# Performance work log

Hardware: AMD Instinct MI355X
Metric: run time of the kernel (lower is better)

Reference implementation:

```python
import jax, jax.numpy as jnp
import numpy as np

B, P = 16, 20480          # scenes, points per scene
N = B * P
FEAT, HID = 128, 128      # FP output channels, head hidden width
CIN = FEAT + 3            # 131 = xyz + features (hard-coded in source: view(..., 131))
GRIPPER_DEPTH = 0.1034
HEADS = (("s", 1), ("z1", 3), ("z2", 3), ("w", 1))


def setup_inputs() -> dict:
    key = jax.random.key(0)
    ks = jax.random.split(key, 2 + 2 * len(HEADS))
    inp = {
        "point_feat": jax.random.normal(ks[0], (N, FEAT), jnp.float32),
        "points": jax.random.normal(ks[1], (N, 3), jnp.float32) * 0.3,
        "batch": jnp.repeat(jnp.arange(B, dtype=jnp.int32), P),
    }
    i = 2
    for name, od in HEADS:
        inp[f"W1_{name}"] = jax.random.normal(ks[i], (HID, CIN), jnp.float32) / np.sqrt(CIN).astype(np.float32)
        inp[f"b1_{name}"] = jnp.zeros((HID,), jnp.float32)
        inp[f"W2_{name}"] = jax.random.normal(ks[i + 1], (od, HID), jnp.float32) / np.sqrt(HID).astype(np.float32)
        inp[f"b2_{name}"] = jnp.zeros((od,), jnp.float32)
        i += 2
    return inp


def _head(x, W1, b1, W2, b2):
    # 1x1 Conv1d stack == per-point MLP: [N,CIN] -> [N,out]
    h = jax.nn.relu(x @ W1.T + b1)
    return h @ W2.T + b2


def _norm(v):
    return v / jnp.linalg.norm(v, axis=1, keepdims=True)


def _forward(point_feat, points,
             W1_s, b1_s, W2_s, b2_s,
             W1_z1, b1_z1, W2_z1, b2_z1,
             W1_z2, b1_z2, W2_z2, b2_z2,
             W1_w, b1_w, W2_w, b2_w):
    pf = jnp.concatenate([points, point_feat], axis=1)          # [N,131]
    s = _head(pf, W1_s, b1_s, W2_s, b2_s)                        # [N,1] (logits)
    z1 = _head(pf, W1_z1, b1_z1, W2_z1, b2_z1)                   # [N,3]
    z2 = _head(pf, W1_z2, b1_z2, W2_z2, b2_z2)                   # [N,3]
    w = _head(pf, W1_w, b1_w, W2_w, b2_w)                        # [N,1]

    # forward() post-processing
    z1 = _norm(z1)
    z2 = z2 - jnp.sum(z1 * z2, axis=-1, keepdims=True) * z1
    z2 = _norm(z2)
    w = jnp.clip(w, -0.08, 0.08)

    # build_6d_grasps, vectorized over all N points
    base = _norm(z1)
    inner = jnp.sum(base * z2, axis=1, keepdims=True)
    approach = (z2 - inner * base) / jnp.linalg.norm(z2, axis=1, keepdims=True)
    base_n = _norm(base)                                          # column 0
    app_n = _norm(approach)                                       # column 2
    grasp_y = _norm(jnp.cross(app_n, base_n))                     # column 1
    trans = points - GRIPPER_DEPTH * app_n + (w / 2.0) * base_n   # column 3
    top = jnp.stack([base_n, grasp_y, app_n, trans], axis=2)      # [N,3,4]
    bottom = jnp.broadcast_to(jnp.array([0.0, 0.0, 0.0, 1.0], jnp.float32), (top.shape[0], 1, 4))
    grasps = jnp.concatenate([top, bottom], axis=1)               # [N,4,4]

    pts_out = points.reshape(B, P, 3)
    grasps_out = grasps.reshape(B, P, 4, 4)
    s_out = s.reshape(B, P)
    w_out = jax.nn.relu(w).reshape(B, P)
    feats_out = pf.reshape(B, P, CIN)
    return pts_out, grasps_out, s_out, w_out, feats_out


def reference(point_feat, points, batch,
              W1_s, b1_s, W2_s, b2_s,
              W1_z1, b1_z1, W2_z1, b2_z1,
              W1_z2, b1_z2, W2_z2, b2_z2,
              W1_w, b1_w, W2_w, b2_w):
    # batch ids only determine num_batches = max(batch)+1 = B (static here)
    return _forward(point_feat, points,
                    W1_s, b1_s, W2_s, b2_s,
                    W1_z1, b1_z1, W2_z1, b2_z1,
                    W1_z2, b1_z2, W2_z2, b2_z2,
                    W1_w, b1_w, W2_w, b2_w)
```

## Files before the change

### kernel.cpp

```cpp
#include <hip/hip_runtime.h>

#define NPTS (16*20480)
#define BM 32
#define NTILES (NPTS/BM)

typedef _Float16 f16;
typedef _Float16 f16x8 __attribute__((ext_vector_type(8)));
typedef float    f32x4 __attribute__((ext_vector_type(4)));

#define O_PTS   ((size_t)0)
#define O_GRASP ((size_t)NPTS*3)
#define O_S     (O_GRASP + (size_t)NPTS*16)
#define O_W     (O_S + (size_t)NPTS)
#define O_FEAT  (O_W + (size_t)NPTS)

struct Params {
  const float* point_feat;
  const float* points;
  const float* W1[4];
  const float* b1[4];
  const float* W2[4];
  const float* b2[4];
  float* out;
};

__launch_bounds__(512, 2)
__global__ void contactnet_fused(Params P)
{
  __shared__ float pf32[BM][132];
  __shared__ float h32[BM][548];
  __shared__ float W2s[8][132];
  __shared__ float b2s[8];
  __shared__ float out2[BM][8][2];
  __shared__ float gr[BM][16];

  const int t    = threadIdx.x;
  const int lane = t & 63;
  const int wv   = t >> 6;
  const int head = wv >> 1;
  const int half = wv & 1;
  const int l15  = lane & 15;
  const int lg   = lane >> 4;

  for (int i = t; i < 8*128; i += 512) {
    int o = i >> 7, k = i & 127;
    int hd = (o + 2) / 3;
    int r  = o - (hd ? 3*hd - 2 : 0);
    W2s[o][k] = P.W2[hd][r*128 + k];
  }
  if (t < 8) {
    int o = t, hd = (o + 2) / 3, r = o - (hd ? 3*hd - 2 : 0);
    b2s[o] = P.b2[hd][r];
  }

  float bias1[4];
  float w1x[4], w1y[4], w1z[4];
  f16x8 Wf_hi[4][4];
  f16x8 Wf_lo[4][4];
  {
    const float* W1h = P.W1[head];
    const float* b1h = P.b1[head];
    #pragma unroll
    for (int nt = 0; nt < 4; ++nt) {
      int row = half*64 + nt*16 + l15;
      const float* wr = W1h + row*131;
      bias1[nt] = b1h[row];
      w1x[nt] = wr[0]; w1y[nt] = wr[1]; w1z[nt] = wr[2];
      #pragma unroll
      for (int kk = 0; kk < 4; ++kk) {
        f16x8 fh, fl;
        int k0 = 3 + kk*32 + lg*8;
        #pragma unroll
        for (int j = 0; j < 8; ++j) {
          float w = wr[k0 + j];
          f16 hi = (f16)w;
          fh[j] = hi;
          fl[j] = (f16)(w - (float)hi);
        }
        Wf_hi[nt][kk] = fh;
        Wf_lo[nt][kk] = fl;
      }
    }
  }

  for (int tile = blockIdx.x; tile < NTILES; tile += gridDim.x) {
    const int base = tile * BM;

    #pragma unroll
    for (int r = 0; r < 2; ++r) {
      int f = t + r*512;
      int p = f >> 5, c4 = f & 31;
      const f32x4 v = *(const f32x4*)(P.point_feat + ((size_t)(base+p)*128 + c4*4));
      *(f32x4*)&pf32[p][c4*4] = v;
      float* dst = P.out + O_FEAT + (size_t)(base+p)*131 + 3 + c4*4;
      dst[0] = v[0]; dst[1] = v[1]; dst[2] = v[2]; dst[3] = v[3];
    }
    if (t < 96) {
      int p = t / 3, c = t - p*3;
      float v = P.points[(size_t)base*3 + t];
      pf32[p][128 + c] = v;
      P.out[O_PTS + (size_t)base*3 + t] = v;
      P.out[O_FEAT + (size_t)(base+p)*131 + c] = v;
    }
    __syncthreads();

    f32x4 acc[2][4];
    #pragma unroll
    for (int mt = 0; mt < 2; ++mt)
      #pragma unroll
      for (int nt = 0; nt < 4; ++nt) {
        acc[mt][nt][0] = bias1[nt]; acc[mt][nt][1] = bias1[nt];
        acc[mt][nt][2] = bias1[nt]; acc[mt][nt][3] = bias1[nt];
      }

    #pragma unroll
    for (int mt = 0; mt < 2; ++mt)
      #pragma unroll
      for (int r = 0; r < 4; ++r) {
        int m = mt*16 + lg*4 + r;
        float x = pf32[m][128], y = pf32[m][129], z = pf32[m][130];
        #pragma unroll
        for (int nt = 0; nt < 4; ++nt)
          acc[mt][nt][r] += x*w1x[nt] + y*w1y[nt] + z*w1z[nt];
      }

    #pragma unroll
    for (int kk = 0; kk < 4; ++kk) {
      f16x8 ah[2], al[2];
      #pragma unroll
      for (int mt = 0; mt < 2; ++mt) {
        int m  = mt*16 + l15;
        int k0 = kk*32 + lg*8;
        f32x4 v0 = *(const f32x4*)&pf32[m][k0];
        f32x4 v1 = *(const f32x4*)&pf32[m][k0+4];
        f16x8 h_, l_;
        #pragma unroll
        for (int j = 0; j < 4; ++j) {
          f16 hi = (f16)v0[j];
          h_[j] = hi; l_[j] = (f16)(v0[j] - (float)hi);
        }
        #pragma unroll
        for (int j = 0; j < 4; ++j) {
          f16 hi = (f16)v1[j];
          h_[4+j] = hi; l_[4+j] = (f16)(v1[j] - (float)hi);
        }
        ah[mt] = h_; al[mt] = l_;
      }
      #pragma unroll
      for (int mt = 0; mt < 2; ++mt)
        #pragma unroll
        for (int nt = 0; nt < 4; ++nt) {
          acc[mt][nt] = __builtin_amdgcn_mfma_f32_16x16x32_f16(ah[mt], Wf_hi[nt][kk], acc[mt][nt], 0, 0, 0);
          acc[mt][nt] = __builtin_amdgcn_mfma_f32_16x16x32_f16(al[mt], Wf_hi[nt][kk], acc[mt][nt], 0, 0, 0);
          acc[mt][nt] = __builtin_amdgcn_mfma_f32_16x16x32_f16(ah[mt], Wf_lo[nt][kk], acc[mt][nt], 0, 0, 0);
        }
    }

    #pragma unroll
    for (int mt = 0; mt < 2; ++mt)
      #pragma unroll
      for (int nt = 0; nt < 4; ++nt)
        #pragma unroll
        for (int r = 0; r < 4; ++r) {
          int prow = mt*16 + lg*4 + r;
          h32[prow][head*136 + half*64 + nt*16 + l15] = fmaxf(acc[mt][nt][r], 0.f);
        }
    __syncthreads();

    {
      int kh = t >> 8;
      int p  = (t >> 3) & 31;
      int o  = t & 7;
      int hd = (o + 2) / 3;
      float a2 = kh ? 0.f : b2s[o];
      const float* hp = &h32[p][hd*136 + kh*64];
      const float* wp = &W2s[o][kh*64];
      #pragma unroll
      for (int i = 0; i < 16; ++i) {
        f32x4 hv = *(const f32x4*)(hp + i*4);
        f32x4 wv = *(const f32x4*)(wp + i*4);
        a2 = fmaf(hv[0], wv[0], a2);
        a2 = fmaf(hv[1], wv[1], a2);
        a2 = fmaf(hv[2], wv[2], a2);
        a2 = fmaf(hv[3], wv[3], a2);
      }
      out2[p][o][kh] = a2;
    }
    __syncthreads();

    if (t < BM) {
      const int p = t;
      float s   = out2[p][0][0] + out2[p][0][1];
      float z1x = out2[p][1][0] + out2[p][1][1];
      float z1y = out2[p][2][0] + out2[p][2][1];
      float z1z = out2[p][3][0] + out2[p][3][1];
      float z2x = out2[p][4][0] + out2[p][4][1];
      float z2y = out2[p][5][0] + out2[p][5][1];
      float z2z = out2[p][6][0] + out2[p][6][1];
      float w   = out2[p][7][0] + out2[p][7][1];
      float px = pf32[p][128], py = pf32[p][129], pz = pf32[p][130];

      float n1 = sqrtf(z1x*z1x + z1y*z1y + z1z*z1z);
      z1x /= n1; z1y /= n1; z1z /= n1;
      float d12 = z1x*z2x + z1y*z2y + z1z*z2z;
      z2x -= d12*z1x; z2y -= d12*z1y; z2z -= d12*z1z;
      float n2 = sqrtf(z2x*z2x + z2y*z2y + z2z*z2z);
      z2x /= n2; z2y /= n2; z2z /= n2;
      w = fminf(fmaxf(w, -0.08f), 0.08f);

      float nb = sqrtf(z1x*z1x + z1y*z1y + z1z*z1z);
      float bx = z1x/nb, by = z1y/nb, bz = z1z/nb;
      float inner = bx*z2x + by*z2y + bz*z2z;
      float na2 = sqrtf(z2x*z2x + z2y*z2y + z2z*z2z);
      float ax = (z2x - inner*bx)/na2, ay = (z2y - inner*by)/na2, az = (z2z - inner*bz)/na2;
      float nbn = sqrtf(bx*bx + by*by + bz*bz);
      float bnx = bx/nbn, bny = by/nbn, bnz = bz/nbn;
      float nan2 = sqrtf(ax*ax + ay*ay + az*az);
      float anx = ax/nan2, any_ = ay/nan2, anz = az/nan2;
      float cx = any_*bnz - anz*bny;
      float cy = anz*bnx - anx*bnz;
      float cz = anx*bny - any_*bnx;
      float nc = sqrtf(cx*cx + cy*cy + cz*cz);
      float gx = cx/nc, gyv = cy/nc, gzv = cz/nc;
      float tx = px - 0.1034f*anx + 0.5f*w*bnx;
      float ty = py - 0.1034f*any_ + 0.5f*w*bny;
      float tz = pz - 0.1034f*anz + 0.5f*w*bnz;

      gr[p][0]=bnx; gr[p][1]=gx;  gr[p][2]=anx;  gr[p][3]=tx;
      gr[p][4]=bny; gr[p][5]=gyv; gr[p][6]=any_; gr[p][7]=ty;
      gr[p][8]=bnz; gr[p][9]=gzv; gr[p][10]=anz; gr[p][11]=tz;
      gr[p][12]=0.f; gr[p][13]=0.f; gr[p][14]=0.f; gr[p][15]=1.f;

      P.out[O_S + base + p] = s;
      P.out[O_W + base + p] = fmaxf(w, 0.f);
    }
    __syncthreads();

    P.out[O_GRASP + (size_t)base*16 + t] = gr[t >> 4][t & 15];
    __syncthreads();
  }
}

extern "C" void kernel_launch(void* const* d_in, const int* in_sizes, int n_in,
                              void* d_out, int out_size, void* d_ws, size_t ws_size,
                              hipStream_t stream) {
  Params P;
  P.point_feat = (const float*)d_in[0];
  P.points     = (const float*)d_in[1];
  int idx = 3;
  for (int h = 0; h < 4; ++h) {
    P.W1[h] = (const float*)d_in[idx + 0];
    P.b1[h] = (const float*)d_in[idx + 1];
    P.W2[h] = (const float*)d_in[idx + 2];
    P.b2[h] = (const float*)d_in[idx + 3];
    idx += 4;
  }
  P.out = (float*)d_out;
  contactnet_fused<<<dim3(512), dim3(512), 0, stream>>>(P);
}
```

Measured before the change: 537.6 us.

## Double-buffer tiles, prefetch next tile, fuse second layer via shuffle reductions

Restructures the fused MLP kernel to 1024-thread blocks on a 256-block grid, with each wave owning 32 hidden units of one head. The next tile's features and points are prefetched from global memory into registers while the current tile is computed, then written into a double-buffered shared f16 hi/lo split. The second layer is computed in registers from the MFMA accumulators with cross-lane shuffle reductions, which removes the shared hidden-activation buffer and one barrier per tile. The costs are higher register pressure under the 1024-thread launch bound, fewer resident blocks, and added shuffle traffic.

```diff
diff --git a/kernel.cpp b/kernel.cpp
--- a/kernel.cpp
+++ b/kernel.cpp
@@ -3,8 +3,10 @@
 #define NPTS (16*20480)
 #define BM 32
 #define NTILES (NPTS/BM)
+#define GRID 256
 
 typedef _Float16 f16;
+typedef _Float16 f16x4 __attribute__((ext_vector_type(4)));
 typedef _Float16 f16x8 __attribute__((ext_vector_type(8)));
 typedef float    f32x4 __attribute__((ext_vector_type(4)));
 
@@ -24,106 +26,113 @@
   float* out;
 };
 
-__launch_bounds__(512, 2)
+__launch_bounds__(1024, 4)
 __global__ void contactnet_fused(Params P)
 {
-  __shared__ float pf32[BM][132];
-  __shared__ float h32[BM][548];
-  __shared__ float W2s[8][132];
+  __shared__ f16   afh[2][BM][136];
+  __shared__ f16   afl[2][BM][136];
+  __shared__ float xyzs[2][BM][3];
+  __shared__ float out2[BM][33];
+  __shared__ float gr[BM][16];
   __shared__ float b2s[8];
-  __shared__ float out2[BM][8][2];
-  __shared__ float gr[BM][16];
 
   const int t    = threadIdx.x;
   const int lane = t & 63;
   const int wv   = t >> 6;
-  const int head = wv >> 1;
-  const int half = wv & 1;
+  const int head = wv >> 2;
+  const int q    = wv & 3;
   const int l15  = lane & 15;
   const int lg   = lane >> 4;
 
-  for (int i = t; i < 8*128; i += 512) {
-    int o = i >> 7, k = i & 127;
-    int hd = (o + 2) / 3;
-    int r  = o - (hd ? 3*hd - 2 : 0);
-    W2s[o][k] = P.W2[hd][r*128 + k];
-  }
-  if (t < 8) {
-    int o = t, hd = (o + 2) / 3, r = o - (hd ? 3*hd - 2 : 0);
-    b2s[o] = P.b2[hd][r];
-  }
-
-  float bias1[4];
-  float w1x[4], w1y[4], w1z[4];
-  f16x8 Wf_hi[4][4];
-  f16x8 Wf_lo[4][4];
+  if (t < 8) { int o = t, hd = (o + 2) / 3, r = o - (hd ? 3*hd - 2 : 0); b2s[o] = P.b2[hd][r]; }
+
+  float bias1[2], w1x[2], w1y[2], w1z[2];
+  f16x8 Whi[2][4], Wlo[2][4];
   {
     const float* W1h = P.W1[head];
     const float* b1h = P.b1[head];
     #pragma unroll
-    for (int nt = 0; nt < 4; ++nt) {
-      int row = half*64 + nt*16 + l15;
+    for (int nt = 0; nt < 2; ++nt) {
+      int row = q*32 + nt*16 + l15;
       const float* wr = W1h + row*131;
       bias1[nt] = b1h[row];
       w1x[nt] = wr[0]; w1y[nt] = wr[1]; w1z[nt] = wr[2];
       #pragma unroll
       for (int kk = 0; kk < 4; ++kk) {
         f16x8 fh, fl;
-        int k0 = 3 + kk*32 + lg*8;
         #pragma unroll
         for (int j = 0; j < 8; ++j) {
-          float w = wr[k0 + j];
+          float w = wr[3 + kk*32 + lg*8 + j];
           f16 hi = (f16)w;
-          fh[j] = hi;
-          fl[j] = (f16)(w - (float)hi);
+          fh[j] = hi; fl[j] = (f16)(w - (float)hi);
         }
-        Wf_hi[nt][kk] = fh;
-        Wf_lo[nt][kk] = fl;
-      }
-    }
-  }
-
-  for (int tile = blockIdx.x; tile < NTILES; tile += gridDim.x) {
+        Whi[nt][kk] = fh; Wlo[nt][kk] = fl;
+      }
+    }
+  }
+  const int goff = (head==0) ? 0 : (head==1) ? 1 : (head==2) ? 4 : 7;
+  const int od   = (head==1 || head==2) ? 3 : 1;
+  float W2r[3][2];
+  #pragma unroll
+  for (int ol = 0; ol < 3; ++ol)
+    #pragma unroll
+    for (int nt = 0; nt < 2; ++nt)
+      W2r[ol][nt] = (ol < od) ? P.W2[head][ol*128 + q*32 + nt*16 + l15] : 0.f;
+
+  const int p_  = t >> 5;
+  const int c4_ = t & 31;
+
+  int tile = blockIdx.x;
+  {
+    f32x4 v = *(const f32x4*)(P.point_feat + ((size_t)(tile*BM + p_)*128 + c4_*4));
+    float xv = (t < 96) ? P.points[(size_t)tile*BM*3 + t] : 0.f;
+    f16x4 hs, ls;
+    #pragma unroll
+    for (int j = 0; j < 4; ++j) { f16 hi = (f16)v[j]; hs[j] = hi; ls[j] = (f16)(v[j] - (float)hi); }
+    *(f16x4*)&afh[0][p_][c4_*4] = hs;
+    *(f16x4*)&afl[0][p_][c4_*4] = ls;
+    float* dst = P.out + O_FEAT + (size_t)(tile*BM + p_)*131 + 3 + c4_*4;
+    dst[0] = v[0]; dst[1] = v[1]; dst[2] = v[2]; dst[3] = v[3];
+    if (t < 96) {
+      int pp = t / 3, c = t - pp*3;
+      xyzs[0][pp][c] = xv;
+      P.out[O_PTS + (size_t)tile*BM*3 + t] = xv;
+      P.out[O_FEAT + (size_t)(tile*BM + pp)*131 + c] = xv;
+    }
+  }
+  __syncthreads();
+
+  int cur = 0;
+  for (;;) {
     const int base = tile * BM;
-
-    #pragma unroll
-    for (int r = 0; r < 2; ++r) {
-      int f = t + r*512;
-      int p = f >> 5, c4 = f & 31;
-      const f32x4 v = *(const f32x4*)(P.point_feat + ((size_t)(base+p)*128 + c4*4));
-      *(f32x4*)&pf32[p][c4*4] = v;
-      float* dst = P.out + O_FEAT + (size_t)(base+p)*131 + 3 + c4*4;
-      dst[0] = v[0]; dst[1] = v[1]; dst[2] = v[2]; dst[3] = v[3];
-    }
-    if (t < 96) {
-      int p = t / 3, c = t - p*3;
-      float v = P.points[(size_t)base*3 + t];
-      pf32[p][128 + c] = v;
-      P.out[O_PTS + (size_t)base*3 + t] = v;
-      P.out[O_FEAT + (size_t)(base+p)*131 + c] = v;
-    }
-    __syncthreads();
-
-    f32x4 acc[2][4];
+    const int nxt  = tile + GRID;
+    const bool has = (nxt < NTILES);
+
+    f32x4 pv = {0,0,0,0};
+    float pxyz = 0.f;
+    if (has) {
+      pv = *(const f32x4*)(P.point_feat + ((size_t)(nxt*BM + p_)*128 + c4_*4));
+      if (t < 96) pxyz = P.points[(size_t)nxt*BM*3 + t];
+    }
+
+    f32x4 acc[2][2];
     #pragma unroll
     for (int mt = 0; mt < 2; ++mt)
       #pragma unroll
-      for (int nt = 0; nt < 4; ++nt) {
+      for (int nt = 0; nt < 2; ++nt) {
         acc[mt][nt][0] = bias1[nt]; acc[mt][nt][1] = bias1[nt];
         acc[mt][nt][2] = bias1[nt]; acc[mt][nt][3] = bias1[nt];
       }
-
     #pragma unroll
     for (int mt = 0; mt < 2; ++mt)
       #pragma unroll
       for (int r = 0; r < 4; ++r) {
         int m = mt*16 + lg*4 + r;
-        float x = pf32[m][128], y = pf32[m][129], z = pf32[m][130];
-        #pragma unroll
-        for (int nt = 0; nt < 4; ++nt)
+        float x = xyzs[cur][m][0], y = xyzs[cur][m][1], z = xyzs[cur][m][2];
+        #pragma unroll
+        for (int nt = 0; nt < 2; ++nt)
           acc[mt][nt][r] += x*w1x[nt] + y*w1y[nt] + z*w1z[nt];
       }
-
     #pragma unroll
     for (int kk = 0; kk < 4; ++kk) {
       f16x8 ah[2], al[2];
@@ -131,74 +140,68 @@
       for (int mt = 0; mt < 2; ++mt) {
         int m  = mt*16 + l15;
         int k0 = kk*32 + lg*8;
-        f32x4 v0 = *(const f32x4*)&pf32[m][k0];
-        f32x4 v1 = *(const f32x4*)&pf32[m][k0+4];
-        f16x8 h_, l_;
-        #pragma unroll
-        for (int j = 0; j < 4; ++j) {
-          f16 hi = (f16)v0[j];
-          h_[j] = hi; l_[j] = (f16)(v0[j] - (float)hi);
+        ah[mt] = *(const f16x8*)&afh[cur][m][k0];
+        al[mt] = *(const f16x8*)&afl[cur][m][k0];
+      }
+      #pragma unroll
+      for (int mt = 0; mt < 2; ++mt)
+        #pragma unroll
+        for (int nt = 0; nt < 2; ++nt) {
+          acc[mt][nt] = __builtin_amdgcn_mfma_f32_16x16x32_f16(ah[mt], Whi[nt][kk], acc[mt][nt], 0, 0, 0);
+          acc[mt][nt] = __builtin_amdgcn_mfma_f32_16x16x32_f16(al[mt], Whi[nt][kk], acc[mt][nt], 0, 0, 0);
+          acc[mt][nt] = __builtin_amdgcn_mfma_f32_16x16x32_f16(ah[mt], Wlo[nt][kk], acc[mt][nt], 0, 0, 0);
         }
-        #pragma unroll
-        for (int j = 0; j < 4; ++j) {
-          f16 hi = (f16)v1[j];
-          h_[4+j] = hi; l_[4+j] = (f16)(v1[j] - (float)hi);
-        }
-        ah[mt] = h_; al[mt] = l_;
-      }
-      #pragma unroll
-      for (int mt = 0; mt < 2; ++mt)
-        #pragma unroll
-        for (int nt = 0; nt < 4; ++nt) {
-          acc[mt][nt] = __builtin_amdgcn_mfma_f32_16x16x32_f16(ah[mt], Wf_hi[nt][kk], acc[mt][nt], 0, 0, 0);
-          acc[mt][nt] = __builtin_amdgcn_mfma_f32_16x16x32_f16(al[mt], Wf_hi[nt][kk], acc[mt][nt], 0, 0, 0);
-          acc[mt][nt] = __builtin_amdgcn_mfma_f32_16x16x32_f16(ah[mt], Wf_lo[nt][kk], acc[mt][nt], 0, 0, 0);
-        }
-    }
-
-    #pragma unroll
-    for (int mt = 0; mt < 2; ++mt)
-      #pragma unroll
-      for (int nt = 0; nt < 4; ++nt)
-        #pragma unroll
-        for (int r = 0; r < 4; ++r) {
-          int prow = mt*16 + lg*4 + r;
-          h32[prow][head*136 + half*64 + nt*16 + l15] = fmaxf(acc[mt][nt][r], 0.f);
-        }
-    __syncthreads();
-
-    {
-      int kh = t >> 8;
-      int p  = (t >> 3) & 31;
-      int o  = t & 7;
-      int hd = (o + 2) / 3;
-      float a2 = kh ? 0.f : b2s[o];
-      const float* hp = &h32[p][hd*136 + kh*64];
-      const float* wp = &W2s[o][kh*64];
-      #pragma unroll
-      for (int i = 0; i < 16; ++i) {
-        f32x4 hv = *(const f32x4*)(hp + i*4);
-        f32x4 wv = *(const f32x4*)(wp + i*4);
-        a2 = fmaf(hv[0], wv[0], a2);
-        a2 = fmaf(hv[1], wv[1], a2);
-        a2 = fmaf(hv[2], wv[2], a2);
-        a2 = fmaf(hv[3], wv[3], a2);
-      }
-      out2[p][o][kh] = a2;
+    }
+
+    #pragma unroll
+    for (int ol = 0; ol < 3; ++ol) {
+      if (ol < od) {
+        #pragma unroll
+        for (int mt = 0; mt < 2; ++mt)
+          #pragma unroll
+          for (int r = 0; r < 4; ++r) {
+            float v = 0.f;
+            #pragma unroll
+            for (int nt = 0; nt < 2; ++nt)
+              v = fmaf(W2r[ol][nt], fmaxf(acc[mt][nt][r], 0.f), v);
+            v += __shfl_xor(v, 1);
+            v += __shfl_xor(v, 2);
+            v += __shfl_xor(v, 4);
+            v += __shfl_xor(v, 8);
+            if (l15 == 0)
+              out2[mt*16 + lg*4 + r][(goff + ol)*4 + q] = v;
+          }
+      }
+    }
+
+    if (has) {
+      f16x4 hs, ls;
+      #pragma unroll
+      for (int j = 0; j < 4; ++j) { f16 hi = (f16)pv[j]; hs[j] = hi; ls[j] = (f16)(pv[j] - (float)hi); }
+      *(f16x4*)&afh[cur^1][p_][c4_*4] = hs;
+      *(f16x4*)&afl[cur^1][p_][c4_*4] = ls;
+      float* dst = P.out + O_FEAT + (size_t)(nxt*BM + p_)*131 + 3 + c4_*4;
+      dst[0] = pv[0]; dst[1] = pv[1]; dst[2] = pv[2]; dst[3] = pv[3];
+      if (t < 96) {
+        int pp = t / 3, c = t - pp*3;
+        xyzs[cur^1][pp][c] = pxyz;
+        P.out[O_PTS + (size_t)nxt*BM*3 + t] = pxyz;
+        P.out[O_FEAT + (size_t)(nxt*BM + pp)*131 + c] = pxyz;
+      }
     }
     __syncthreads();
 
     if (t < BM) {
       const int p = t;
-      float s   = out2[p][0][0] + out2[p][0][1];
-      float z1x = out2[p][1][0] + out2[p][1][1];
-      float z1y = out2[p][2][0] + out2[p][2][1];
-      float z1z = out2[p][3][0] + out2[p][3][1];
-      float z2x = out2[p][4][0] + out2[p][4][1];
-      float z2y = out2[p][5][0] + out2[p][5][1];
-      float z2z = out2[p][6][0] + out2[p][6][1];
-      float w   = out2[p][7][0] + out2[p][7][1];
-      float px = pf32[p][128], py = pf32[p][129], pz = pf32[p][130];
+      float o_[8];
+      #pragma unroll
+      for (int o = 0; o < 8; ++o)
+        o_[o] = b2s[o] + out2[p][o*4+0] + out2[p][o*4+1] + out2[p][o*4+2] + out2[p][o*4+3];
+      float s = o_[0];
+      float z1x = o_[1], z1y = o_[2], z1z = o_[3];
+      float z2x = o_[4], z2y = o_[5], z2z = o_[6];
+      float w   = o_[7];
+      float px = xyzs[cur][p][0], py = xyzs[cur][p][1], pz = xyzs[cur][p][2];
 
       float n1 = sqrtf(z1x*z1x + z1y*z1y + z1z*z1z);
       z1x /= n1; z1y /= n1; z1z /= n1;
@@ -236,8 +239,11 @@
     }
     __syncthreads();
 
-    P.out[O_GRASP + (size_t)base*16 + t] = gr[t >> 4][t & 15];
-    __syncthreads();
+    if (t < 512)
+      P.out[O_GRASP + (size_t)base*16 + t] = gr[t >> 4][t & 15];
+
+    if (!has) break;
+    tile = nxt; cur ^= 1;
   }
 }
 
@@ -256,5 +262,5 @@
     idx += 4;
   }
   P.out = (float*)d_out;
-  contactnet_fused<<<dim3(512), dim3(512), 0, stream>>>(P);
+  contactnet_fused<<<dim3(GRID), dim3(1024), 0, stream>>>(P);
 }
```

Result: slower. 714.0 us (+32.8%).
